# Performance work log

Hardware: AMD Instinct MI355X
Metric: run time of the kernel (lower is better)

The kernel has to match this reference:

```python
import jax, jax.numpy as jnp
import numpy as np

D_MODEL, N_HEADS, D_HEAD, D_FF, N_LAYERS, VOCAB = 768, 12, 64, 3072, 4, 32000
B, S = 4, 1024
EPS = 1e-5
NEG = -1000000000.0


def layer_norm(x, gamma, beta):
    mean = jnp.mean(x, axis=-1, keepdims=True)
    var = jnp.mean((x - mean) ** 2, axis=-1, keepdims=True)
    return gamma * ((x - mean) / jnp.sqrt(var + EPS)) + beta


def gelu_lean(x):
    return x * (0.5 * (1.0 + jnp.tanh(0.7978845608 * (x + 0.044715 * x * x * x))))


def positional_encoding(seq_len, dim, dtype):
    idx = jnp.arange(dim)
    exponent = (2 * (idx // 2)).astype(dtype) / float(dim)
    pos = jnp.arange(seq_len, dtype=dtype)[:, None]
    angle = pos / jnp.power(jnp.asarray(10000.0, dtype), exponent[None, :])
    return jnp.where((idx % 2 == 0)[None, :], jnp.sin(angle), jnp.cos(angle))


def setup_inputs() -> dict:
    key = jax.random.key(0)
    ks = jax.random.split(key, 10)
    std = 0.02
    inp = {
        "tokens": jax.random.randint(ks[0], (B, S), 0, VOCAB),
        "predict_idx": 1023,
        "embedding": std * jax.random.normal(ks[1], (D_MODEL, VOCAB), jnp.float32),
        "ln1_g": jnp.ones((N_LAYERS, D_MODEL), jnp.float32),
        "ln1_b": jnp.zeros((N_LAYERS, D_MODEL), jnp.float32),
        "wq": std * jax.random.normal(ks[2], (N_LAYERS, N_HEADS, D_HEAD, D_MODEL), jnp.float32),
        "wk": std * jax.random.normal(ks[3], (N_LAYERS, N_HEADS, D_HEAD, D_MODEL), jnp.float32),
        "wv": std * jax.random.normal(ks[4], (N_LAYERS, N_HEADS, D_HEAD, D_MODEL), jnp.float32),
        "wo": std * jax.random.normal(ks[5], (N_LAYERS, D_MODEL, N_HEADS * D_HEAD), jnp.float32),
        "ln2_g": jnp.ones((N_LAYERS, D_MODEL), jnp.float32),
        "ln2_b": jnp.zeros((N_LAYERS, D_MODEL), jnp.float32),
        "fc1": std * jax.random.normal(ks[6], (N_LAYERS, D_FF, D_MODEL), jnp.float32),
        "fc2": std * jax.random.normal(ks[7], (N_LAYERS, D_MODEL, D_FF), jnp.float32),
        "lnf_g": jnp.ones((D_MODEL,), jnp.float32),
        "lnf_b": jnp.zeros((D_MODEL,), jnp.float32),
        "unembed": std * jax.random.normal(ks[8], (VOCAB, D_MODEL), jnp.float32),
    }
    return inp


def reference(tokens, predict_idx, embedding, ln1_g, ln1_b, wq, wk, wv, wo,
              ln2_g, ln2_b, fc1, fc2, lnf_g, lnf_b, unembed):
    dtype = embedding.dtype
    b, s = tokens.shape
    d_head = wq.shape[2]
    scale = 1.0 / float(np.sqrt(d_head))

    # token embedding [B,S,D] + sinusoidal positions
    x = embedding.T[tokens] + positional_encoding(s, embedding.shape[0], dtype)[None]

    # causal mask: True above the diagonal -> filled with -1e9
    causal = jnp.triu(jnp.ones((s, s), bool), k=1)

    for l in range(wq.shape[0]):
        h = layer_norm(x, ln1_g[l], ln1_b[l])
        q = jnp.einsum('bsd,hed->bhse', h, wq[l])
        k = jnp.einsum('bsd,hed->bhse', h, wk[l])
        v = jnp.einsum('bsd,hed->bhse', h, wv[l])
        scores = jnp.einsum('bhse,bhte->bhst', q, k) * scale
        scores = jnp.where(causal[None, None], NEG, scores)
        weights = jax.nn.softmax(scores, axis=-1)
        attn = jnp.einsum('bhst,bhte->bhse', weights, v)  # [B,H,S,dh]
        attn = attn.transpose(0, 2, 1, 3).reshape(b, s, -1)  # concat heads
        x = x + attn @ wo[l].T
        h2 = layer_norm(x, ln2_g[l], ln2_b[l])
        x = x + gelu_lean(h2 @ fc1[l].T) @ fc2[l].T

    selected = x[:, predict_idx, :]  # [B, D]
    normed = layer_norm(selected, lnf_g, lnf_b)
    return normed @ unembed.T  # [B, vocab]
```

## Files before the change

### kernel.cpp

```cpp
#include <hip/hip_runtime.h>
#include <hip/hip_bf16.h>

#define D_MODEL 768
#define N_HEADS 12
#define D_HEAD  64
#define D_FF    3072
#define N_LAYERS 4
#define VOCAB   32000
#define BATCH   4
#define SEQ     1024
#define NROWS   (BATCH*SEQ)
#define NEGV    -1000000000.0f
#define LN_EPS  1e-5f

typedef __attribute__((ext_vector_type(8))) short bf16x8;
typedef __attribute__((ext_vector_type(4))) float f32x4;
typedef __attribute__((ext_vector_type(8))) unsigned short u16x8;
typedef __attribute__((ext_vector_type(4))) unsigned short u16x4;

typedef __attribute__((address_space(1))) const unsigned int g_u32;
typedef __attribute__((address_space(3))) unsigned int l_u32;

__device__ __forceinline__ float bf2f(unsigned short u) {
  return __uint_as_float(((unsigned int)u) << 16);
}
__device__ __forceinline__ unsigned short f2bf(float f) {
  __hip_bfloat16 h = __float2bfloat16(f);
  return *reinterpret_cast<unsigned short*>(&h);
}

__device__ __forceinline__ float block_reduce_sum(float v, float* sbuf) {
#pragma unroll
  for (int off = 32; off > 0; off >>= 1) v += __shfl_down(v, off, 64);
  int lane = threadIdx.x & 63, wid = threadIdx.x >> 6;
  if (lane == 0) sbuf[wid] = v;
  __syncthreads();
  if (threadIdx.x == 0) sbuf[4] = sbuf[0] + sbuf[1] + sbuf[2] + sbuf[3];
  __syncthreads();
  return sbuf[4];
}

__device__ __forceinline__ float gelu_f(float x) {
  float c = x + 0.044715f * x * x * x;
  return x * (0.5f * (1.0f + tanhf(0.7978845608f * c)));
}

__global__ __launch_bounds__(256) void convert_kernel(
    const float* __restrict__ src, __hip_bfloat16* __restrict__ dst, int n)
{
  int i = (blockIdx.x * 256 + threadIdx.x) * 8;
  if (i >= n) return;
  float4 a = *(const float4*)(src + i);
  float4 b = *(const float4*)(src + i + 4);
  struct bf8 { __hip_bfloat16 h[8]; } r;
  r.h[0] = __float2bfloat16(a.x); r.h[1] = __float2bfloat16(a.y);
  r.h[2] = __float2bfloat16(a.z); r.h[3] = __float2bfloat16(a.w);
  r.h[4] = __float2bfloat16(b.x); r.h[5] = __float2bfloat16(b.y);
  r.h[6] = __float2bfloat16(b.z); r.h[7] = __float2bfloat16(b.w);
  *(bf8*)(dst + i) = r;
}

__global__ __launch_bounds__(256) void qkv_pack_kernel(
    const float* __restrict__ wq, const float* __restrict__ wk,
    const float* __restrict__ wv, __hip_bfloat16* __restrict__ dst)
{
  const int WMAT = D_MODEL * D_MODEL;
  long long i = (long long)(blockIdx.x * 256 + threadIdx.x) * 8;
  long long l = i / (3LL * WMAT);
  long long rem = i - l * 3LL * WMAT;
  int which = (int)(rem / WMAT);
  long long off = rem - (long long)which * WMAT;
  const float* src = (which == 0 ? wq : which == 1 ? wk : wv) + l * WMAT + off;
  float4 a = *(const float4*)src;
  float4 b = *(const float4*)(src + 4);
  struct bf8 { __hip_bfloat16 h[8]; } r;
  r.h[0] = __float2bfloat16(a.x); r.h[1] = __float2bfloat16(a.y);
  r.h[2] = __float2bfloat16(a.z); r.h[3] = __float2bfloat16(a.w);
  r.h[4] = __float2bfloat16(b.x); r.h[5] = __float2bfloat16(b.y);
  r.h[6] = __float2bfloat16(b.z); r.h[7] = __float2bfloat16(b.w);
  *(bf8*)(dst + i) = r;
}

__global__ __launch_bounds__(256) void transpose_emb_kernel(
    const float* __restrict__ emb, __hip_bfloat16* __restrict__ embT)
{
  __shared__ float tile[64][65];
  const int vb = blockIdx.x * 64;
  const int db = blockIdx.y * 64;
  const int tid = threadIdx.x;
  {
    int r = tid >> 4, c = (tid & 15) * 4;
#pragma unroll
    for (int p = 0; p < 4; ++p) {
      float4 v = *(const float4*)(emb + (size_t)(db + r + p * 16) * VOCAB + vb + c);
      tile[c + 0][r + p * 16] = v.x;
      tile[c + 1][r + p * 16] = v.y;
      tile[c + 2][r + p * 16] = v.z;
      tile[c + 3][r + p * 16] = v.w;
    }
  }
  __syncthreads();
  {
    int v = tid >> 2, d0 = (tid & 3) * 16;
    unsigned short* op = (unsigned short*)embT + (size_t)(vb + v) * D_MODEL + db + d0;
    u16x8 o0, o1;
#pragma unroll
    for (int j = 0; j < 8; ++j) {
      o0[j] = f2bf(tile[v][d0 + j]);
      o1[j] = f2bf(tile[v][d0 + 8 + j]);
    }
    *(u16x8*)op = o0;
    *(u16x8*)(op + 8) = o1;
  }
}

__global__ __launch_bounds__(256) void embed_kernel(
    const int* __restrict__ tokens, const __hip_bfloat16* __restrict__ embT,
    float* __restrict__ x)
{
  int bs = blockIdx.x;
  int s = bs & (SEQ - 1);
  int tok = tokens[bs];
  const unsigned short* ep = (const unsigned short*)embT + (size_t)tok * D_MODEL;
  for (int d = threadIdx.x; d < D_MODEL; d += 256) {
    float ev = bf2f(ep[d]);
    int dpair = d & ~1;
    float expo = (float)dpair * (1.0f / (float)D_MODEL);
    float ang = (float)s / powf(10000.0f, expo);
    float pe = (d & 1) ? cosf(ang) : sinf(ang);
    x[(size_t)bs * D_MODEL + d] = ev + pe;
  }
}

__global__ __launch_bounds__(256) void ln_kernel(
    const float* __restrict__ in, __hip_bfloat16* __restrict__ out,
    const float* __restrict__ g, const float* __restrict__ bb)
{
  __shared__ float sbuf[8];
  size_t row = blockIdx.x;
  const float* rp = in + row * D_MODEL;
  int t = threadIdx.x;
  float x0 = rp[t], x1 = rp[t + 256], x2 = rp[t + 512];
  float mean = block_reduce_sum(x0 + x1 + x2, sbuf) * (1.0f / (float)D_MODEL);
  float d0 = x0 - mean, d1 = x1 - mean, d2 = x2 - mean;
  float var = block_reduce_sum(d0*d0 + d1*d1 + d2*d2, sbuf) * (1.0f / (float)D_MODEL);
  float rstd = rsqrtf(var + LN_EPS);
  __hip_bfloat16* op = out + row * D_MODEL;
  op[t]       = __float2bfloat16(g[t]       * (d0 * rstd) + bb[t]);
  op[t + 256] = __float2bfloat16(g[t + 256] * (d1 * rstd) + bb[t + 256]);
  op[t + 512] = __float2bfloat16(g[t + 512] * (d2 * rstd) + bb[t + 512]);
}

__global__ __launch_bounds__(256) void final_ln_kernel(
    const float* __restrict__ x, const int* __restrict__ pidx,
    const float* __restrict__ g, const float* __restrict__ bb,
    float* __restrict__ out)
{
  __shared__ float sbuf[8];
  int p = pidx[0];
  const float* rp = x + ((size_t)blockIdx.x * SEQ + p) * D_MODEL;
  int t = threadIdx.x;
  float x0 = rp[t], x1 = rp[t + 256], x2 = rp[t + 512];
  float mean = block_reduce_sum(x0 + x1 + x2, sbuf) * (1.0f / (float)D_MODEL);
  float d0 = x0 - mean, d1 = x1 - mean, d2 = x2 - mean;
  float var = block_reduce_sum(d0*d0 + d1*d1 + d2*d2, sbuf) * (1.0f / (float)D_MODEL);
  float rstd = rsqrtf(var + LN_EPS);
  float* op = out + (size_t)blockIdx.x * D_MODEL;
  op[t]       = g[t]       * (d0 * rstd) + bb[t];
  op[t + 256] = g[t + 256] * (d1 * rstd) + bb[t + 256];
  op[t + 512] = g[t + 512] * (d2 * rstd) + bb[t + 512];
}

__device__ __forceinline__ int2 xcd_tile(int gx, int gy) {
  int flat = blockIdx.y * gx + blockIdx.x;
  int cpx = (gx * gy) >> 3;
  int logical = (flat & 7) * cpx + (flat >> 3);
  return make_int2(logical % gx, logical / gx);
}

#define WAITV4() asm volatile("s_waitcnt vmcnt(4)" ::: "memory")
#define WAITV0() asm volatile("s_waitcnt vmcnt(0)" ::: "memory")
#define MEMFENCE() asm volatile("" ::: "memory")

__global__ __launch_bounds__(256) void gemm_bf16_kernel(
    const __hip_bfloat16* __restrict__ A, const __hip_bfloat16* __restrict__ W,
    void* __restrict__ Cv, const float* __restrict__ resid,
    int N, int K, int mode)
{
  __shared__ __align__(16) unsigned short As[3][128 * 32];
  __shared__ __align__(16) unsigned short Bs[3][128 * 32];
  const unsigned short* Au = (const unsigned short*)A;
  const unsigned short* Wu = (const unsigned short*)W;
  const int tid = threadIdx.x;
  const int wv = tid >> 6, ln = tid & 63;
  const int l15 = ln & 15, l4 = ln >> 4;
  int2 tc = xcd_tile(N >> 7, gridDim.y);
  const int bm = tc.y * 128, bn = tc.x * 128;
  const int wr = wv >> 1, wc = wv & 1;

  const int lrow = wv * 16 + (ln >> 2);
  const int schunk = (ln & 3) ^ ((ln >> 3) & 3);
  const size_t gA0 = (size_t)(bm + lrow) * K + schunk * 8;
  const size_t gA1 = (size_t)(bm + 64 + lrow) * K + schunk * 8;
  const size_t gB0 = (size_t)(bn + lrow) * K + schunk * 8;
  const size_t gB1 = (size_t)(bn + 64 + lrow) * K + schunk * 8;
  const int ldsb = wv * 512;

#define STAGE128(buf, k0)                                                          \
  {                                                                                \
    __builtin_amdgcn_global_load_lds((g_u32*)(Au + gA0 + (k0)), (l_u32*)(As[buf] + ldsb), 16, 0, 0);        \
    __builtin_amdgcn_global_load_lds((g_u32*)(Au + gA1 + (k0)), (l_u32*)(As[buf] + 2048 + ldsb), 16, 0, 0); \
    __builtin_amdgcn_global_load_lds((g_u32*)(Wu + gB0 + (k0)), (l_u32*)(Bs[buf] + ldsb), 16, 0, 0);        \
    __builtin_amdgcn_global_load_lds((g_u32*)(Wu + gB1 + (k0)), (l_u32*)(Bs[buf] + 2048 + ldsb), 16, 0, 0); \
  }

  const int rslot = (l4 ^ ((l15 >> 1) & 3)) * 8;

#define COMPUTE128(buf)                                                            \
  {                                                                                \
    bf16x8 af[4], bfr[4];                                                          \
    _Pragma("unroll")                                                              \
    for (int m = 0; m < 4; ++m)                                                    \
      af[m] = *(const bf16x8*)(As[buf] + (wr * 64 + m * 16 + l15) * 32 + rslot);   \
    _Pragma("unroll")                                                              \
    for (int n = 0; n < 4; ++n)                                                    \
      bfr[n] = *(const bf16x8*)(Bs[buf] + (wc * 64 + n * 16 + l15) * 32 + rslot);  \
    __builtin_amdgcn_s_setprio(1);                                                 \
    _Pragma("unroll")                                                              \
    for (int m = 0; m < 4; ++m)                                                    \
      _Pragma("unroll")                                                            \
      for (int n = 0; n < 4; ++n)                                                  \
        acc[m][n] = __builtin_amdgcn_mfma_f32_16x16x32_bf16(af[m], bfr[n], acc[m][n], 0, 0, 0); \
    __builtin_amdgcn_s_setprio(0);                                                 \
  }

  f32x4 acc[4][4];
#pragma unroll
  for (int m = 0; m < 4; ++m)
#pragma unroll
    for (int n = 0; n < 4; ++n) acc[m][n] = (f32x4){0.f, 0.f, 0.f, 0.f};

  const int NT = K >> 5;
  STAGE128(0, 0);
  STAGE128(1, 32);
  int cur = 0;
  for (int t = 0; t < NT - 1; ++t) {
    WAITV4();
    __builtin_amdgcn_s_barrier();
    MEMFENCE();
    if (t + 2 < NT) {
      int nxt = cur + 2; if (nxt >= 3) nxt -= 3;
      STAGE128(nxt, (t + 2) << 5);
    }
    COMPUTE128(cur);
    cur = (cur == 2) ? 0 : cur + 1;
  }
  WAITV0();
  __builtin_amdgcn_s_barrier();
  MEMFENCE();
  COMPUTE128(cur);

  float* Cf = (float*)Cv;
  __hip_bfloat16* Cb = (__hip_bfloat16*)Cv;
#pragma unroll
  for (int m = 0; m < 4; ++m) {
#pragma unroll
    for (int n = 0; n < 4; ++n) {
#pragma unroll
      for (int r = 0; r < 4; ++r) {
        int row = bm + wr * 64 + m * 16 + l4 * 4 + r;
        int col = bn + wc * 64 + n * 16 + l15;
        size_t off = (size_t)row * N + col;
        float v = acc[m][n][r];
        if (mode == 0)      Cf[off] = v;
        else if (mode == 1) Cf[off] = v + resid[off];
        else if (mode == 2) Cb[off] = __float2bfloat16(v);
        else                Cb[off] = __float2bfloat16(gelu_f(v));
      }
    }
  }
#undef STAGE128
#undef COMPUTE128
}

__global__ __launch_bounds__(256) void gemm64_bf16_kernel(
    const __hip_bfloat16* __restrict__ A, const __hip_bfloat16* __restrict__ W,
    void* __restrict__ Cv, const float* __restrict__ resid,
    int N, int K, int mode)
{
  __shared__ __align__(16) unsigned short As[3][64 * 64];
  __shared__ __align__(16) unsigned short Bs[3][64 * 64];
  const unsigned short* Au = (const unsigned short*)A;
  const unsigned short* Wu = (const unsigned short*)W;
  const int tid = threadIdx.x;
  const int wv = tid >> 6, ln = tid & 63;
  const int l15 = ln & 15, l4 = ln >> 4;
  int2 tc = xcd_tile(N >> 6, gridDim.y);
  const int bm = tc.y * 64, bn = tc.x * 64;
  const int wr = wv >> 1, wc = wv & 1;

  const int srow = tid >> 3;
  const int schunk = (tid & 7) ^ ((tid >> 3) & 7);
  const size_t gA0 = (size_t)(bm + srow) * K + schunk * 8;
  const size_t gA1 = (size_t)(bm + 32 + srow) * K + schunk * 8;
  const size_t gB0 = (size_t)(bn + srow) * K + schunk * 8;
  const size_t gB1 = (size_t)(bn + 32 + srow) * K + schunk * 8;
  const int ldsb = wv * 512;

#define STAGE64(buf, k0)                                                           \
  {                                                                                \
    __builtin_amdgcn_global_load_lds((g_u32*)(Au + gA0 + (k0)), (l_u32*)(As[buf] + ldsb), 16, 0, 0);        \
    __builtin_amdgcn_global_load_lds((g_u32*)(Au + gA1 + (k0)), (l_u32*)(As[buf] + 2048 + ldsb), 16, 0, 0); \
    __builtin_amdgcn_global_load_lds((g_u32*)(Wu + gB0 + (k0)), (l_u32*)(Bs[buf] + ldsb), 16, 0, 0);        \
    __builtin_amdgcn_global_load_lds((g_u32*)(Wu + gB1 + (k0)), (l_u32*)(Bs[buf] + 2048 + ldsb), 16, 0, 0); \
  }

#define COMPUTE64(buf)                                                             \
  {                                                                                \
    bf16x8 af[2][2], bfr[2][2];                                                    \
    _Pragma("unroll")                                                              \
    for (int ks = 0; ks < 2; ++ks) {                                               \
      _Pragma("unroll")                                                            \
      for (int m = 0; m < 2; ++m)                                                  \
        af[ks][m] = *(const bf16x8*)(As[buf] + (wr * 32 + m * 16 + l15) * 64 +     \
                                     (((ks * 4 + l4) ^ (l15 & 7)) << 3));          \
      _Pragma("unroll")                                                            \
      for (int n = 0; n < 2; ++n)                                                  \
        bfr[ks][n] = *(const bf16x8*)(Bs[buf] + (wc * 32 + n * 16 + l15) * 64 +    \
                                      (((ks * 4 + l4) ^ (l15 & 7)) << 3));         \
    }                                                                              \
    __builtin_amdgcn_s_setprio(1);                                                 \
    _Pragma("unroll")                                                              \
    for (int ks = 0; ks < 2; ++ks)                                                 \
      _Pragma("unroll")                                                            \
      for (int m = 0; m < 2; ++m)                                                  \
        _Pragma("unroll")                                                          \
        for (int n = 0; n < 2; ++n)                                                \
          acc[m][n] = __builtin_amdgcn_mfma_f32_16x16x32_bf16(af[ks][m], bfr[ks][n], acc[m][n], 0, 0, 0); \
    __builtin_amdgcn_s_setprio(0);                                                 \
  }

  f32x4 acc[2][2];
#pragma unroll
  for (int m = 0; m < 2; ++m)
#pragma unroll
    for (int n = 0; n < 2; ++n) acc[m][n] = (f32x4){0.f, 0.f, 0.f, 0.f};

  const int NT = K >> 6;
  STAGE64(0, 0);
  STAGE64(1, 64);
  int cur = 0;
  for (int t = 0; t < NT - 1; ++t) {
    WAITV4();
    __builtin_amdgcn_s_barrier();
    MEMFENCE();
    if (t + 2 < NT) {
      int nxt = cur + 2; if (nxt >= 3) nxt -= 3;
      STAGE64(nxt, (t + 2) << 6);
    }
    COMPUTE64(cur);
    cur = (cur == 2) ? 0 : cur + 1;
  }
  WAITV0();
  __builtin_amdgcn_s_barrier();
  MEMFENCE();
  COMPUTE64(cur);

  float* Cf = (float*)Cv;
  __hip_bfloat16* Cb = (__hip_bfloat16*)Cv;
#pragma unroll
  for (int m = 0; m < 2; ++m) {
#pragma unroll
    for (int n = 0; n < 2; ++n) {
#pragma unroll
      for (int r = 0; r < 4; ++r) {
        int row = bm + wr * 32 + m * 16 + l4 * 4 + r;
        int col = bn + wc * 32 + n * 16 + l15;
        size_t off = (size_t)row * N + col;
        float v = acc[m][n][r];
        if (mode == 0)      Cf[off] = v;
        else if (mode == 1) Cf[off] = v + resid[off];
        else if (mode == 2) Cb[off] = __float2bfloat16(v);
        else                Cb[off] = __float2bfloat16(gelu_f(v));
      }
    }
  }
#undef STAGE64
#undef COMPUTE64
}

__global__ __launch_bounds__(128) void flash_attn_kernel(
    const __hip_bfloat16* __restrict__ qkv_, __hip_bfloat16* __restrict__ attn_)
{
  const unsigned short* qkv = (const unsigned short*)qkv_;
  unsigned short* attn = (unsigned short*)attn_;
  const int px = blockIdx.x;
  const int h  = blockIdx.y;
  const int b  = blockIdx.z;
  const int tid = threadIdx.x;
  const int wq = tid >> 6, ln = tid & 63;
  const int l15 = ln & 15, l4 = ln >> 4;

  __shared__ unsigned short Ks[2][64 * 64];
  __shared__ unsigned short Vt[2][64 * 64];
  __shared__ unsigned short Pw[2][16 * 64];

  const int krow = tid >> 3;
  const int kchunk = (tid & 7) ^ ((tid >> 3) & 7);
  const int kldsbase = (tid & 64) * 8;

  const int vc = tid & 7;
  const int vp = tid >> 3;
  const int vtr = (2 * vp) & 7;
  const int vtb0 = vp >> 2;

  u16x8 v0, v1, v2, v3;

#define STAGE_K(buf, t0)                                                           \
  {                                                                                \
    _Pragma("unroll")                                                              \
    for (int j = 0; j < 4; ++j) {                                                  \
      const unsigned short* gk = qkv +                                             \
          (size_t)(b * SEQ + (t0) + j * 16 + krow) * 2304 + 768 + h * 64 + kchunk * 8; \
      __builtin_amdgcn_global_load_lds((g_u32*)gk,                                 \
          (l_u32*)(Ks[buf] + j * 1024 + kldsbase), 16, 0, 0);                      \
    }                                                                              \
  }

#define LOAD_V(t0)                                                                 \
  {                                                                                \
    const unsigned short* gv = qkv +                                               \
        (size_t)(b * SEQ + (t0) + 2 * vp) * 2304 + 1536 + h * 64 + vc * 8;         \
    v0 = *(const u16x8*)gv;                                                        \
    v1 = *(const u16x8*)(gv + 2304);                                               \
    v2 = *(const u16x8*)(gv + 32 * 2304);                                          \
    v3 = *(const u16x8*)(gv + 33 * 2304);                                          \
  }

#define WRITE_VT(buf)                                                              \
  {                                                                                \
    _Pragma("unroll")                                                              \
    for (int j = 0; j < 8; ++j) {                                                  \
      int e = vc * 8 + j;                                                          \
      unsigned int w01 = (unsigned int)(unsigned short)v0[j] |                     \
                         ((unsigned int)(unsigned short)v1[j] << 16);              \
      unsigned int w23 = (unsigned int)(unsigned short)v2[j] |                     \
                         ((unsigned int)(unsigned short)v3[j] << 16);              \
      *(unsigned int*)(Vt[buf] + e * 64 + ((vtb0 ^ (e & 7)) << 3) + vtr) = w01;    \
      *(unsigned int*)(Vt[buf] + e * 64 + (((vtb0 + 4) ^ (e & 7)) << 3) + vtr) = w23; \
    }                                                                              \
  }

  for (int pass = 0; pass < 2; ++pass) {
    const int qi = (pass == 0) ? px : 31 - px;
    const int s0 = qi * 32;
    const int ntiles = (qi >> 1) + 1;
    const int qg = s0 + wq * 16 + l15;

    bf16x8 qf[2];
    {
      const size_t qbase = (size_t)(b * SEQ + qg) * 2304 + h * 64;
#pragma unroll
      for (int ks = 0; ks < 2; ++ks) {
        u16x8 raw = *(const u16x8*)(qkv + qbase + ks * 32 + l4 * 8);
        bf16x8 q;
#pragma unroll
        for (int j = 0; j < 8; ++j) q[j] = (short)f2bf(bf2f(raw[j]) * 0.125f);
        qf[ks] = q;
      }
    }

    float mrow = -1e30f, lrow = 0.f;
    f32x4 o[4];
#pragma unroll
    for (int n = 0; n < 4; ++n) o[n] = (f32x4){0.f, 0.f, 0.f, 0.f};

    STAGE_K(0, 0);
    LOAD_V(0);
    WAITV0();
    WRITE_VT(0);
    __syncthreads();

    for (int t = 0; t < ntiles; ++t) {
      const int cur = t & 1;
      const bool pfn = (t + 1 < ntiles);
      if (pfn) { STAGE_K(cur ^ 1, (t + 1) * 64); LOAD_V((t + 1) * 64); }

      f32x4 sf[4];
#pragma unroll
      for (int n = 0; n < 4; ++n) sf[n] = (f32x4){0.f, 0.f, 0.f, 0.f};
#pragma unroll
      for (int ks = 0; ks < 2; ++ks) {
#pragma unroll
        for (int n = 0; n < 4; ++n) {
          int tr = n * 16 + l15;
          bf16x8 kf = *(const bf16x8*)(Ks[cur] + tr * 64 + (((ks * 4 + l4) ^ (tr & 7)) << 3));
          sf[n] = __builtin_amdgcn_mfma_f32_16x16x32_bf16(kf, qf[ks], sf[n], 0, 0, 0);
        }
      }

      if (t == ntiles - 1) {
#pragma unroll
        for (int n = 0; n < 4; ++n) {
#pragma unroll
          for (int r = 0; r < 4; ++r) {
            int tg = t * 64 + n * 16 + l4 * 4 + r;
            if (tg > qg) sf[n][r] = NEGV;
          }
        }
      }

      float mx = sf[0][0];
#pragma unroll
      for (int n = 0; n < 4; ++n)
#pragma unroll
        for (int r = 0; r < 4; ++r) mx = fmaxf(mx, sf[n][r]);
      mx = fmaxf(mx, __shfl_xor(mx, 16));
      mx = fmaxf(mx, __shfl_xor(mx, 32));
      float mnew = fmaxf(mrow, mx);
      float alpha = __expf(mrow - mnew);
      float pb[4][4];
      float sum = 0.f;
#pragma unroll
      for (int n = 0; n < 4; ++n)
#pragma unroll
        for (int r = 0; r < 4; ++r) {
          float p = __expf(sf[n][r] - mnew);
          pb[n][r] = p;
          sum += p;
        }
      sum += __shfl_xor(sum, 16);
      sum += __shfl_xor(sum, 32);
      lrow = lrow * alpha + sum;
      mrow = mnew;

      float ar[4];
#pragma unroll
      for (int r = 0; r < 4; ++r)
        ar[r] = __shfl(alpha, (ln & 48) | (l4 * 4 + r));
#pragma unroll
      for (int n = 0; n < 4; ++n)
#pragma unroll
        for (int r = 0; r < 4; ++r) o[n][r] *= ar[r];

      unsigned short* Pme = Pw[wq];
#pragma unroll
      for (int n = 0; n < 4; ++n) {
        int tb = 2 * n + (l4 >> 1);
        u16x4 w;
        w[0] = f2bf(pb[n][0]); w[1] = f2bf(pb[n][1]);
        w[2] = f2bf(pb[n][2]); w[3] = f2bf(pb[n][3]);
        *(u16x4*)(Pme + l15 * 64 + ((tb ^ (l15 & 7)) << 3) + (l4 & 1) * 4) = w;
      }

#pragma unroll
      for (int ks = 0; ks < 2; ++ks) {
        bf16x8 pf = *(const bf16x8*)(Pme + l15 * 64 + (((ks * 4 + l4) ^ (l15 & 7)) << 3));
#pragma unroll
        for (int n = 0; n < 4; ++n) {
          int e = n * 16 + l15;
          bf16x8 vf = *(const bf16x8*)(Vt[cur] + e * 64 + (((ks * 4 + l4) ^ (e & 7)) << 3));
          o[n] = __builtin_amdgcn_mfma_f32_16x16x32_bf16(pf, vf, o[n], 0, 0, 0);
        }
      }

      if (pfn) { WAITV0(); WRITE_VT(cur ^ 1); }
      __syncthreads();
    }

    float lr[4];
#pragma unroll
    for (int r = 0; r < 4; ++r)
      lr[r] = __shfl(lrow, (ln & 48) | (l4 * 4 + r));
#pragma unroll
    for (int r = 0; r < 4; ++r) {
      float inv = 1.0f / lr[r];
      size_t base = (size_t)(b * SEQ + s0 + wq * 16 + l4 * 4 + r) * D_MODEL + h * 64;
#pragma unroll
      for (int n = 0; n < 4; ++n)
        attn[base + n * 16 + l15] = f2bf(o[n][r] * inv);
    }
  }
#undef STAGE_K
#undef LOAD_V
#undef WRITE_VT
}

__global__ __launch_bounds__(256) void logits_kernel(
    const float* __restrict__ normed, const float* __restrict__ unemb,
    float* __restrict__ out)
{
  __shared__ __align__(16) float ns[BATCH][D_MODEL];
  for (int d = threadIdx.x; d < BATCH * D_MODEL; d += 256)
    ((float*)ns)[d] = normed[d];
  __syncthreads();
  int g = threadIdx.x >> 4, li = threadIdx.x & 15;
  int v = blockIdx.x * 16 + g;
  const float* up = unemb + (size_t)v * D_MODEL;
  float s0 = 0.f, s1 = 0.f, s2 = 0.f, s3 = 0.f;
#pragma unroll
  for (int it = 0; it < D_MODEL / 64; ++it) {
    int e = it * 64 + li * 4;
    float4 u = *(const float4*)(up + e);
    float4 n0 = *(const float4*)&ns[0][e];
    float4 n1 = *(const float4*)&ns[1][e];
    float4 n2 = *(const float4*)&ns[2][e];
    float4 n3 = *(const float4*)&ns[3][e];
    s0 += u.x*n0.x + u.y*n0.y + u.z*n0.z + u.w*n0.w;
    s1 += u.x*n1.x + u.y*n1.y + u.z*n1.z + u.w*n1.w;
    s2 += u.x*n2.x + u.y*n2.y + u.z*n2.z + u.w*n2.w;
    s3 += u.x*n3.x + u.y*n3.y + u.z*n3.z + u.w*n3.w;
  }
#pragma unroll
  for (int msk = 1; msk < 16; msk <<= 1) {
    s0 += __shfl_xor(s0, msk, 64); s1 += __shfl_xor(s1, msk, 64);
    s2 += __shfl_xor(s2, msk, 64); s3 += __shfl_xor(s3, msk, 64);
  }
  if (li == 0) {
    out[(size_t)0 * VOCAB + v] = s0;
    out[(size_t)1 * VOCAB + v] = s1;
    out[(size_t)2 * VOCAB + v] = s2;
    out[(size_t)3 * VOCAB + v] = s3;
  }
}

extern "C" void kernel_launch(void* const* d_in, const int* in_sizes, int n_in,
                              void* d_out, int out_size, void* d_ws, size_t ws_size,
                              hipStream_t stream) {
  const int*   tokens = (const int*)d_in[0];
  const int*   pidx   = (const int*)d_in[1];
  const float* emb    = (const float*)d_in[2];
  const float* ln1_g  = (const float*)d_in[3];
  const float* ln1_b  = (const float*)d_in[4];
  const float* wq     = (const float*)d_in[5];
  const float* wk     = (const float*)d_in[6];
  const float* wv     = (const float*)d_in[7];
  const float* wo     = (const float*)d_in[8];
  const float* ln2_g  = (const float*)d_in[9];
  const float* ln2_b  = (const float*)d_in[10];
  const float* fc1    = (const float*)d_in[11];
  const float* fc2    = (const float*)d_in[12];
  const float* lnf_g  = (const float*)d_in[13];
  const float* lnf_b  = (const float*)d_in[14];
  const float* unemb  = (const float*)d_in[15];
  float* out = (float*)d_out;

  char* wp = (char*)d_ws;
  const size_t NX = (size_t)NROWS * D_MODEL;
  float* x = (float*)wp;                  wp += NX * 4;
  float* normed = (float*)wp;             wp += BATCH * D_MODEL * 4;
  __hip_bfloat16* h    = (__hip_bfloat16*)wp; wp += NX * 2;
  __hip_bfloat16* attn = (__hip_bfloat16*)wp; wp += NX * 2;
  __hip_bfloat16* qkvb = (__hip_bfloat16*)wp; wp += (size_t)NROWS * 2304 * 2;
  __hip_bfloat16* ffn  = (__hip_bfloat16*)wp; wp += (size_t)NROWS * D_FF * 2;
  __hip_bfloat16* wqkvb = (__hip_bfloat16*)wp; wp += (size_t)N_LAYERS * 2304 * D_MODEL * 2;
  __hip_bfloat16* wob   = (__hip_bfloat16*)wp; wp += (size_t)N_LAYERS * D_MODEL * D_MODEL * 2;
  __hip_bfloat16* fc1b  = (__hip_bfloat16*)wp; wp += (size_t)N_LAYERS * D_FF * D_MODEL * 2;
  __hip_bfloat16* fc2b  = (__hip_bfloat16*)wp; wp += (size_t)N_LAYERS * D_MODEL * D_FF * 2;

  __hip_bfloat16* embT = attn;

  const int WMAT = D_MODEL * D_MODEL;
  const int FMAT = D_FF * D_MODEL;

  transpose_emb_kernel<<<dim3(VOCAB / 64, D_MODEL / 64), 256, 0, stream>>>(emb, embT);
  embed_kernel<<<NROWS, 256, 0, stream>>>(tokens, embT, x);

  qkv_pack_kernel<<<N_LAYERS * 3 * WMAT / 2048, 256, 0, stream>>>(wq, wk, wv, wqkvb);
  convert_kernel<<<N_LAYERS * WMAT / 2048, 256, 0, stream>>>(wo,  wob,  N_LAYERS * WMAT);
  convert_kernel<<<N_LAYERS * FMAT / 2048, 256, 0, stream>>>(fc1, fc1b, N_LAYERS * FMAT);
  convert_kernel<<<N_LAYERS * FMAT / 2048, 256, 0, stream>>>(fc2, fc2b, N_LAYERS * FMAT);

  for (int l = 0; l < N_LAYERS; ++l) {
    const size_t qofs = (size_t)l * 3 * WMAT;
    const size_t wofs = (size_t)l * WMAT;
    const size_t fofs = (size_t)l * FMAT;

    ln_kernel<<<NROWS, 256, 0, stream>>>(x, h, ln1_g + l * D_MODEL, ln1_b + l * D_MODEL);

    gemm_bf16_kernel<<<dim3(2304 / 128, NROWS / 128), 256, 0, stream>>>(
        h, wqkvb + qofs, qkvb, nullptr, 2304, D_MODEL, 2);

    flash_attn_kernel<<<dim3(16, N_HEADS, BATCH), 128, 0, stream>>>(qkvb, attn);

    gemm64_bf16_kernel<<<dim3(D_MODEL / 64, NROWS / 64), 256, 0, stream>>>(
        attn, wob + wofs, x, x, D_MODEL, D_MODEL, 1);

    ln_kernel<<<NROWS, 256, 0, stream>>>(x, h, ln2_g + l * D_MODEL, ln2_b + l * D_MODEL);

    gemm_bf16_kernel<<<dim3(D_FF / 128, NROWS / 128), 256, 0, stream>>>(
        h, fc1b + fofs, ffn, nullptr, D_FF, D_MODEL, 3);

    gemm64_bf16_kernel<<<dim3(D_MODEL / 64, NROWS / 64), 256, 0, stream>>>(
        ffn, fc2b + fofs, x, x, D_MODEL, D_FF, 1);
  }

  final_ln_kernel<<<BATCH, 256, 0, stream>>>(x, pidx, lnf_g, lnf_b, normed);
  logits_kernel<<<VOCAB / 16, 256, 0, stream>>>(normed, unemb, out);
}
```

Measured before the change: 807.5 us.

## Merge weight conversions, use exp-based GELU, and raise MFMA priority in attention

Replaces the three fp32-to-bf16 conversion launches for wo/fc1/fc2 with a single kernel that writes into the contiguous wob/fc1b/fc2b region. Rewrites the tanh GELU as the algebraically equivalent x*sigmoid(2z) form using a fast __expf. Wraps the QK and PV MFMA loops in flash attention with s_setprio so matrix work is favoured over other wavefronts. This saves launch overhead and transcendental cost, but relies on the bf16 weight buffers being laid out contiguously, and the priority hints may not help scheduling.

```diff
diff --git a/kernel.cpp b/kernel.cpp
--- a/kernel.cpp
+++ b/kernel.cpp
@@ -41,23 +41,8 @@
 }
 
 __device__ __forceinline__ float gelu_f(float x) {
-  float c = x + 0.044715f * x * x * x;
-  return x * (0.5f * (1.0f + tanhf(0.7978845608f * c)));
-}
-
-__global__ __launch_bounds__(256) void convert_kernel(
-    const float* __restrict__ src, __hip_bfloat16* __restrict__ dst, int n)
-{
-  int i = (blockIdx.x * 256 + threadIdx.x) * 8;
-  if (i >= n) return;
-  float4 a = *(const float4*)(src + i);
-  float4 b = *(const float4*)(src + i + 4);
-  struct bf8 { __hip_bfloat16 h[8]; } r;
-  r.h[0] = __float2bfloat16(a.x); r.h[1] = __float2bfloat16(a.y);
-  r.h[2] = __float2bfloat16(a.z); r.h[3] = __float2bfloat16(a.w);
-  r.h[4] = __float2bfloat16(b.x); r.h[5] = __float2bfloat16(b.y);
-  r.h[6] = __float2bfloat16(b.z); r.h[7] = __float2bfloat16(b.w);
-  *(bf8*)(dst + i) = r;
+  float z2 = 1.5957691216f * x * (1.0f + 0.044715f * x * x);
+  return x / (1.0f + __expf(-z2));
 }
 
 __global__ __launch_bounds__(256) void qkv_pack_kernel(
@@ -71,6 +56,27 @@
   int which = (int)(rem / WMAT);
   long long off = rem - (long long)which * WMAT;
   const float* src = (which == 0 ? wq : which == 1 ? wk : wv) + l * WMAT + off;
+  float4 a = *(const float4*)src;
+  float4 b = *(const float4*)(src + 4);
+  struct bf8 { __hip_bfloat16 h[8]; } r;
+  r.h[0] = __float2bfloat16(a.x); r.h[1] = __float2bfloat16(a.y);
+  r.h[2] = __float2bfloat16(a.z); r.h[3] = __float2bfloat16(a.w);
+  r.h[4] = __float2bfloat16(b.x); r.h[5] = __float2bfloat16(b.y);
+  r.h[6] = __float2bfloat16(b.z); r.h[7] = __float2bfloat16(b.w);
+  *(bf8*)(dst + i) = r;
+}
+
+__global__ __launch_bounds__(256) void convert3_kernel(
+    const float* __restrict__ wo, const float* __restrict__ fc1,
+    const float* __restrict__ fc2, __hip_bfloat16* __restrict__ dst)
+{
+  const long long WM4 = 4LL * D_MODEL * D_MODEL;
+  const long long FM4 = 4LL * D_FF * D_MODEL;
+  long long i = (long long)(blockIdx.x * 256 + threadIdx.x) * 8;
+  const float* src;
+  if (i < WM4)            src = wo  + i;
+  else if (i < WM4 + FM4) src = fc1 + (i - WM4);
+  else                    src = fc2 + (i - WM4 - FM4);
   float4 a = *(const float4*)src;
   float4 b = *(const float4*)(src + 4);
   struct bf8 { __hip_bfloat16 h[8]; } r;
@@ -489,6 +495,7 @@
       f32x4 sf[4];
 #pragma unroll
       for (int n = 0; n < 4; ++n) sf[n] = (f32x4){0.f, 0.f, 0.f, 0.f};
+      __builtin_amdgcn_s_setprio(1);
 #pragma unroll
       for (int ks = 0; ks < 2; ++ks) {
 #pragma unroll
@@ -498,6 +505,7 @@
           sf[n] = __builtin_amdgcn_mfma_f32_16x16x32_bf16(kf, qf[ks], sf[n], 0, 0, 0);
         }
       }
+      __builtin_amdgcn_s_setprio(0);
 
       if (t == ntiles - 1) {
 #pragma unroll
@@ -553,6 +561,7 @@
         *(u16x4*)(Pme + l15 * 64 + ((tb ^ (l15 & 7)) << 3) + (l4 & 1) * 4) = w;
       }
 
+      __builtin_amdgcn_s_setprio(1);
 #pragma unroll
       for (int ks = 0; ks < 2; ++ks) {
         bf16x8 pf = *(const bf16x8*)(Pme + l15 * 64 + (((ks * 4 + l4) ^ (l15 & 7)) << 3));
@@ -563,6 +572,7 @@
           o[n] = __builtin_amdgcn_mfma_f32_16x16x32_bf16(pf, vf, o[n], 0, 0, 0);
         }
       }
+      __builtin_amdgcn_s_setprio(0);
 
       if (pfn) { WAITV0(); WRITE_VT(cur ^ 1); }
       __syncthreads();
@@ -667,9 +677,7 @@
   embed_kernel<<<NROWS, 256, 0, stream>>>(tokens, embT, x);
 
   qkv_pack_kernel<<<N_LAYERS * 3 * WMAT / 2048, 256, 0, stream>>>(wq, wk, wv, wqkvb);
-  convert_kernel<<<N_LAYERS * WMAT / 2048, 256, 0, stream>>>(wo,  wob,  N_LAYERS * WMAT);
-  convert_kernel<<<N_LAYERS * FMAT / 2048, 256, 0, stream>>>(fc1, fc1b, N_LAYERS * FMAT);
-  convert_kernel<<<N_LAYERS * FMAT / 2048, 256, 0, stream>>>(fc2, fc2b, N_LAYERS * FMAT);
+  convert3_kernel<<<(N_LAYERS * (WMAT + 2 * FMAT)) / 2048, 256, 0, stream>>>(wo, fc1, fc2, wob);
 
   for (int l = 0; l < N_LAYERS; ++l) {
     const size_t qofs = (size_t)l * 3 * WMAT;
```

Result: faster. 785.7 us (median of 2 runs) (-2.7%).
